# Kernel tuning notes

Measured on AMD Instinct MI355X. Metric: run time of the kernel, lower is better.

The kernel has to match this reference:

```python
import jax, jax.numpy as jnp
import numpy as np

P = 7            # cfg.POOLING_SIZE (= group_size)
N_CLASSES = 21   # PASCAL VOC incl. background
SPATIAL_SCALE = 1.0 / 16.0


def _round_half_up(x):
    # matches C round() for non-negative roi coords (jnp.round is banker's)
    return jnp.floor(x + 0.5)


def psroi_pool(feat, rois, out_dim):
    """Position-sensitive RoI average pooling via integral images.
    feat: [B, out_dim*P*P, H, W]; rois: [N, 5] (batch_idx, x1, y1, x2, y2).
    Returns [N, out_dim, P, P]."""
    B, C, H, W = feat.shape
    # summed-area table, zero-padded: S[b,c,h,w] = sum feat[b,c,:h,:w]
    S = jnp.cumsum(jnp.cumsum(feat, axis=2), axis=3)
    S = jnp.pad(S, ((0, 0), (0, 0), (1, 0), (1, 0)))

    b = rois[:, 0].astype(jnp.int32)
    x1 = _round_half_up(rois[:, 1]) * SPATIAL_SCALE
    y1 = _round_half_up(rois[:, 2]) * SPATIAL_SCALE
    x2 = _round_half_up(rois[:, 3] + 1.0) * SPATIAL_SCALE
    y2 = _round_half_up(rois[:, 4] + 1.0) * SPATIAL_SCALE
    roi_w = jnp.maximum(x2 - x1, 0.1)
    roi_h = jnp.maximum(y2 - y1, 0.1)
    bin_w = roi_w / P
    bin_h = roi_h / P

    g = jnp.arange(P, dtype=feat.dtype)
    hs = jnp.clip(jnp.floor(g[None] * bin_h[:, None] + y1[:, None]), 0, H).astype(jnp.int32)        # [N,P]
    he = jnp.clip(jnp.ceil((g[None] + 1.0) * bin_h[:, None] + y1[:, None]), 0, H).astype(jnp.int32)
    ws = jnp.clip(jnp.floor(g[None] * bin_w[:, None] + x1[:, None]), 0, W).astype(jnp.int32)
    we = jnp.clip(jnp.ceil((g[None] + 1.0) * bin_w[:, None] + x1[:, None]), 0, W).astype(jnp.int32)

    # channel for (ctop, gh, gw) is (ctop*P + gh)*P + gw == arange(C) reshaped
    c = jnp.arange(C, dtype=jnp.int32).reshape(1, out_dim, P, P)
    bi = b[:, None, None, None]
    h0 = hs[:, None, :, None]; h1 = he[:, None, :, None]
    w0 = ws[:, None, None, :]; w1 = we[:, None, None, :]
    # box-sum from integral image -> [N, out_dim, P, P]
    ssum = S[bi, c, h1, w1] - S[bi, c, h0, w1] - S[bi, c, h1, w0] + S[bi, c, h0, w0]

    dh = jnp.maximum(he - hs, 0)[:, None, :, None]
    dw = jnp.maximum(we - ws, 0)[:, None, None, :]
    area = (dh * dw).astype(feat.dtype)
    return jnp.where(area > 0, ssum / jnp.maximum(area, 1.0), 0.0)


def setup_inputs() -> dict:
    key = jax.random.key(0)
    k1, k2, k3, k4, k5 = jax.random.split(key, 5)
    B, Cin, H, W = 4, 2048, 64, 64
    base_feat = jax.random.normal(k1, (B, Cin, H, W), jnp.float32)
    w_conv1 = 0.01 * jax.random.normal(k2, (1024, Cin), jnp.float32)
    w_cls = 0.01 * jax.random.normal(k3, (N_CLASSES * P * P, 1024), jnp.float32)
    w_bbox = 0.001 * jax.random.normal(k4, (4 * N_CLASSES * P * P, 1024), jnp.float32)
    # 300 ROIs per image in image coords (image size = 16*H = 1024)
    n_per = 300
    ka, kb = jax.random.split(k5)
    xy1 = jax.random.uniform(ka, (B * n_per, 2), jnp.float32, 0.0, 900.0)
    wh = jax.random.uniform(kb, (B * n_per, 2), jnp.float32, 16.0, 160.0)
    xy2 = jnp.minimum(xy1 + wh, 1023.0)
    bidx = jnp.repeat(jnp.arange(B, dtype=jnp.float32), n_per)[:, None]
    rois = jnp.concatenate([bidx, xy1[:, 0:1], xy1[:, 1:2], xy2[:, 0:1], xy2[:, 1:2]], axis=1)
    return {"base_feat": base_feat, "rois": rois, "w_conv1": w_conv1, "w_cls": w_cls, "w_bbox": w_bbox}


def reference(base_feat, rois, w_conv1, w_cls, w_bbox):
    B = base_feat.shape[0]
    n_per = rois.shape[0] // B
    # 1x1 conv (no bias) + relu
    x = jax.nn.relu(jnp.einsum('oi,bihw->bohw', w_conv1, base_feat))
    # cls branch: 1x1 conv -> PSRoIPool -> PxP avgpool -> softmax
    cls_feat = jnp.einsum('oi,bihw->bohw', w_cls, x)
    pooled_cls = psroi_pool(cls_feat, rois, N_CLASSES)        # [N, 21, P, P]
    cls_score = pooled_cls.mean(axis=(2, 3))                   # [N, 21]
    cls_prob = jax.nn.softmax(cls_score, axis=1)
    # bbox branch: 1x1 conv -> PSRoIPool -> PxP avgpool
    bbox_feat = jnp.einsum('oi,bihw->bohw', w_bbox, x)
    pooled_loc = psroi_pool(bbox_feat, rois, 4 * N_CLASSES)    # [N, 84, P, P]
    bbox_pred = pooled_loc.mean(axis=(2, 3))                    # [N, 84]
    return cls_prob.reshape(B, n_per, -1), bbox_pred.reshape(B, n_per, -1)
```

## Files before the change

kernel.cpp:

```cpp
#include <hip/hip_runtime.h>
#include <cstdint>


typedef __attribute__((ext_vector_type(8))) short short8;
typedef __attribute__((ext_vector_type(4))) short short4v;
typedef __attribute__((ext_vector_type(4))) float f32x4;

#define OFF_FEATT 0ull
#define OFF_W1    67108864ull
#define OFF_U2    0ull
#define OFF_P2    64225280ull
#define OFF_WC    71303168ull
#define OFF_DESC  84148224ull
#define OFF_SCORE 86155264ull
#define OFF_X     86810624ull
#define OFF_U1    153919488ull
#define OFF_P1    282370048ull
#define ONEPASS_BYTES 296419328ull

__device__ __forceinline__ unsigned short f2bf(float f) {
  unsigned u = __float_as_uint(f);
  u += 0x7fffu + ((u >> 16) & 1u);
  return (unsigned short)(u >> 16);
}
__device__ __forceinline__ float bf2f(unsigned short h) {
  return __uint_as_float(((unsigned)h) << 16);
}

__device__ __forceinline__ int swz6(int k6, int key) {
  return ((((k6 >> 3) & 7) ^ key) << 3) | (k6 & 7);
}

__device__ __forceinline__ void gload16(const void* g, void* l) {
  __builtin_amdgcn_global_load_lds((const __attribute__((address_space(1))) void*)g,
                                   (__attribute__((address_space(3))) void*)l, 16, 0, 0);
}

__global__ __launch_bounds__(256) void k_cvt_w1(const float* __restrict__ src,
                                                unsigned short* __restrict__ dst) {
  int t = blockIdx.x * 256 + threadIdx.x;
  long e = (long)t * 4;
  if (e >= 1024 * 2048) return;
  int o = (int)(e >> 11), k = (int)(e & 2047);
  float4 q = *(const float4*)(src + e);
  short4v s = {(short)f2bf(q.x), (short)f2bf(q.y), (short)f2bf(q.z), (short)f2bf(q.w)};
  int kp = (k & ~63) | swz6(k & 63, o & 7);
  *(short4v*)(dst + (size_t)o * 2048 + kp) = s;
}

__global__ __launch_bounds__(256) void k_cvt_wcomb(const float* __restrict__ wcls,
                                                   const float* __restrict__ wbbox,
                                                   unsigned short* __restrict__ dst) {
  int t = blockIdx.x * 256 + threadIdx.x;
  if (t >= 128 * 49 * 256) return;
  size_t e = (size_t)t * 4;
  int c = (int)(e / 50176);
  int rem = (int)(e - (size_t)c * 50176);
  int ij = rem >> 10, k = rem & 1023;
  float4 q = make_float4(0.f, 0.f, 0.f, 0.f);
  if (c < 21)       q = *(const float4*)(wcls + (size_t)(c * 49 + ij) * 1024 + k);
  else if (c < 105) q = *(const float4*)(wbbox + (size_t)((c - 21) * 49 + ij) * 1024 + k);
  short4v s = {(short)f2bf(q.x), (short)f2bf(q.y), (short)f2bf(q.z), (short)f2bf(q.w)};
  int kp = (k & ~63) | swz6(k & 63, c & 7);
  *(short4v*)(dst + ((size_t)(c * 49 + ij) * 1024 + kp)) = s;
}

__global__ __launch_bounds__(256) void k_tpose(const float* __restrict__ src,
                                               unsigned short* __restrict__ dst) {
  __shared__ float tile[64][65];
  int s0 = blockIdx.x * 64, c0 = blockIdx.y * 64, b = blockIdx.z;
  int tx = threadIdx.x & 63, ty = threadIdx.x >> 6;
  const float* sp = src + ((size_t)b * 2048 + c0) * 4096 + s0;
#pragma unroll
  for (int i = 0; i < 16; i++) {
    int cl = ty * 16 + i;
    tile[cl][tx] = sp[(size_t)cl * 4096 + tx];
  }
  __syncthreads();
  unsigned short* dp = dst + ((size_t)b * 4096 + s0) * 2048 + c0;
  int c4 = (threadIdx.x & 15) * 4;
  int sy = threadIdx.x >> 4;
#pragma unroll
  for (int i = 0; i < 4; i++) {
    int sl = i * 16 + sy;
    int key = sl & 7;
    short4v v = {(short)f2bf(tile[c4 + 0][sl]), (short)f2bf(tile[c4 + 1][sl]),
                 (short)f2bf(tile[c4 + 2][sl]), (short)f2bf(tile[c4 + 3][sl])};
    *(short4v*)(dp + (size_t)sl * 2048 + swz6(c4, key)) = v;
  }
}

__global__ __launch_bounds__(256) void k_gemm_conv1(const short* __restrict__ A,
                                                    const short* __restrict__ Bw,
                                                    float* __restrict__ X) {
  int mt = blockIdx.x, nt = blockIdx.y, b = blockIdx.z;
  __shared__ short As[128 * 64];
  __shared__ short Bs[128 * 64];
  int tid = threadIdx.x, lane = tid & 63, wave = tid >> 6;
  int wm = wave >> 1, wn = wave & 1;
  f32x4 acc[4][4];
#pragma unroll
  for (int i = 0; i < 4; i++)
#pragma unroll
    for (int j = 0; j < 4; j++) acc[i][j] = (f32x4){0.f, 0.f, 0.f, 0.f};

  const short* Ab = A + ((size_t)b * 4096 + (size_t)mt * 128) * 2048;
  const short* Bb = Bw + (size_t)nt * 128 * 2048;
  int lr = lane >> 3;
  int lc = (lane & 7) * 8;
  int key = lane & 7;

  for (int k0 = 0; k0 < 2048; k0 += 64) {
#pragma unroll
    for (int i = 0; i < 4; i++) {
      int row = i * 32 + wave * 8 + lr;
      gload16(Ab + (size_t)row * 2048 + k0 + lc, (char*)As + (i * 32 + wave * 8) * 128);
      gload16(Bb + (size_t)row * 2048 + k0 + lc, (char*)Bs + (i * 32 + wave * 8) * 128);
    }
    __syncthreads();
#pragma unroll
    for (int kt = 0; kt < 2; kt++) {
      int ko = (((kt << 2) | (lane >> 4)) ^ key) << 3;
      short8 af[4], bfr[4];
#pragma unroll
      for (int i = 0; i < 4; i++)
        af[i] = *(const short8*)(As + (wm * 64 + i * 16 + (lane & 15)) * 64 + ko);
#pragma unroll
      for (int j = 0; j < 4; j++)
        bfr[j] = *(const short8*)(Bs + (wn * 64 + j * 16 + (lane & 15)) * 64 + ko);
#pragma unroll
      for (int i = 0; i < 4; i++)
#pragma unroll
        for (int j = 0; j < 4; j++)
          acc[i][j] = __builtin_amdgcn_mfma_f32_16x16x32_bf16(af[i], bfr[j], acc[i][j], 0, 0, 0);
    }
    __syncthreads();
  }
  float* Xb = X + ((size_t)b * 4096 + (size_t)mt * 128) * 1024 + nt * 128;
#pragma unroll
  for (int i = 0; i < 4; i++)
#pragma unroll
    for (int j = 0; j < 4; j++) {
      int row = wm * 64 + i * 16 + (lane >> 4) * 4;
      int col = wn * 64 + j * 16 + (lane & 15);
#pragma unroll
      for (int r = 0; r < 4; r++)
        Xb[(size_t)(row + r) * 1024 + col] = fmaxf(acc[i][j][r], 0.f);
    }
}

__global__ __launch_bounds__(256) void k_desc(const float* __restrict__ rois,
                                              int* __restrict__ desc) {
  int t = blockIdx.x * 256 + threadIdx.x;
  if (t >= 1280 * 49) return;
  int roi = t / 49, ij = t - roi * 49;
  int* d = desc + (size_t)t * 8;
  if (roi >= 1200) { d[0] = 0; d[1] = 0; d[2] = 0; d[3] = 0; d[4] = 0; ((float*)d)[5] = 0.f; return; }
  const float* r = rois + (size_t)roi * 5;
  int b = (int)r[0];
  float x1 = __fmul_rn(floorf(__fadd_rn(r[1], 0.5f)), 0.0625f);
  float y1 = __fmul_rn(floorf(__fadd_rn(r[2], 0.5f)), 0.0625f);
  float x2 = __fmul_rn(floorf(__fadd_rn(__fadd_rn(r[3], 1.0f), 0.5f)), 0.0625f);
  float y2 = __fmul_rn(floorf(__fadd_rn(__fadd_rn(r[4], 1.0f), 0.5f)), 0.0625f);
  float bw = __fdiv_rn(fmaxf(__fsub_rn(x2, x1), 0.1f), 7.0f);
  float bh = __fdiv_rn(fmaxf(__fsub_rn(y2, y1), 0.1f), 7.0f);
  int i = ij / 7, j = ij - (ij / 7) * 7;
  float fi = (float)i, fj = (float)j;
  int hs = (int)fminf(fmaxf(floorf(__fadd_rn(__fmul_rn(fi, bh), y1)), 0.f), 64.f);
  int he = (int)fminf(fmaxf(ceilf(__fadd_rn(__fmul_rn(__fadd_rn(fi, 1.f), bh), y1)), 0.f), 64.f);
  int wsx = (int)fminf(fmaxf(floorf(__fadd_rn(__fmul_rn(fj, bw), x1)), 0.f), 64.f);
  int we = (int)fminf(fmaxf(ceilf(__fadd_rn(__fmul_rn(__fadd_rn(fj, 1.f), bw), x1)), 0.f), 64.f);
  int dh = max(he - hs, 0), dw = max(we - wsx, 0);
  float inv = (dh * dw > 0) ? 1.0f / (float)(dh * dw) : 0.f;
  d[0] = b; d[1] = hs; d[2] = he; d[3] = wsx; d[4] = we;
  ((float*)d)[5] = inv;
}

__global__ __launch_bounds__(256) void k_ubuild(const float* __restrict__ X,
                                                const int* __restrict__ desc,
                                                unsigned short* __restrict__ U) {
  int t = blockIdx.x;
  const int* d = desc + (size_t)t * 8;
  int b = d[0], hs = d[1], he = d[2], wsx = d[3], we = d[4];
  float inv = ((const float*)d)[5];
  int key = (t / 49) & 7;
  int k = threadIdx.x * 4;
  float ax = 0.f, ay = 0.f, az = 0.f, aw = 0.f;
  for (int h = hs; h < he; h++) {
    const float* rowp = X + ((size_t)((b * 64 + h) * 64 + wsx)) * 1024 + k;
    for (int w = wsx; w < we; w++) {
      float4 q = *(const float4*)rowp;
      ax += q.x; ay += q.y; az += q.z; aw += q.w;
      rowp += 1024;
    }
  }
  short4v s = {(short)f2bf(ax * inv), (short)f2bf(ay * inv),
               (short)f2bf(az * inv), (short)f2bf(aw * inv)};
  int kp = (k & ~63) | swz6(k & 63, key);
  *(short4v*)(U + (size_t)t * 1024 + kp) = s;
}

__global__ __launch_bounds__(256) void k_poolgemm2(const unsigned short* __restrict__ U,
                                                   const unsigned short* __restrict__ Wc,
                                                   unsigned short* __restrict__ P,
                                                   int nroi) {
  int mt = blockIdx.x;
  int ij = blockIdx.y;
  __shared__ short As[64 * 64];
  __shared__ short Bs[128 * 64];
  int tid = threadIdx.x, lane = tid & 63, wave = tid >> 6;
  f32x4 acc[4][2];
#pragma unroll
  for (int i = 0; i < 4; i++)
#pragma unroll
    for (int j = 0; j < 2; j++) acc[i][j] = (f32x4){0.f, 0.f, 0.f, 0.f};

  const unsigned short* Ab = U + ((size_t)mt * 64 * 49 + ij) * 1024;
  const unsigned short* Bb = Wc + (size_t)ij * 1024;
  int lr = lane >> 3, lc = (lane & 7) * 8;
  int key = lane & 7;

  for (int k0 = 0; k0 < 1024; k0 += 64) {
#pragma unroll
    for (int i = 0; i < 2; i++) {
      int row = i * 32 + wave * 8 + lr;
      gload16(Ab + (size_t)row * (49 * 1024) + k0 + lc, (char*)As + (i * 32 + wave * 8) * 128);
    }
#pragma unroll
    for (int i = 0; i < 4; i++) {
      int row = i * 32 + wave * 8 + lr;
      gload16(Bb + (size_t)row * (49 * 1024) + k0 + lc, (char*)Bs + (i * 32 + wave * 8) * 128);
    }
    __syncthreads();
#pragma unroll
    for (int kt = 0; kt < 2; kt++) {
      int ko = (((kt << 2) | (lane >> 4)) ^ key) << 3;
      short8 af[4], bfr[2];
#pragma unroll
      for (int i = 0; i < 4; i++)
        af[i] = *(const short8*)(As + (i * 16 + (lane & 15)) * 64 + ko);
#pragma unroll
      for (int j = 0; j < 2; j++)
        bfr[j] = *(const short8*)(Bs + (wave * 32 + j * 16 + (lane & 15)) * 64 + ko);
#pragma unroll
      for (int i = 0; i < 4; i++)
#pragma unroll
        for (int j = 0; j < 2; j++)
          acc[i][j] = __builtin_amdgcn_mfma_f32_16x16x32_bf16(af[i], bfr[j], acc[i][j], 0, 0, 0);
    }
    __syncthreads();
  }
  unsigned short* Pb = P + (size_t)ij * nroi * 112;
#pragma unroll
  for (int i = 0; i < 4; i++)
#pragma unroll
    for (int j = 0; j < 2; j++) {
      int cc = wave * 32 + j * 16 + (lane & 15);
      if (cc < 112) {
        int rbase = mt * 64 + i * 16 + (lane >> 4) * 4;
#pragma unroll
        for (int r = 0; r < 4; r++)
          Pb[(size_t)(rbase + r) * 112 + cc] = f2bf(acc[i][j][r]);
      }
    }
}

__global__ __launch_bounds__(256) void k_reduce(const unsigned short* __restrict__ P,
                                                float* __restrict__ score, int nroi) {
  int t = blockIdx.x * 256 + threadIdx.x;
  if (t >= nroi * 112) return;
  int roi = t / 112, c = t - roi * 112;
  float s = 0.f;
#pragma unroll 7
  for (int ij = 0; ij < 49; ij++) s += bf2f(P[(size_t)ij * nroi * 112 + t]);
  score[(size_t)roi * 128 + c] = s;
}

__global__ __launch_bounds__(256) void k_final(const float* __restrict__ score,
                                               float* __restrict__ out) {
  int t = blockIdx.x * 256 + threadIdx.x;
  if (t < 1200) {
    float s[21];
    float mx = -1e30f;
#pragma unroll
    for (int c = 0; c < 21; c++) {
      s[c] = score[(size_t)t * 128 + c] * (1.f / 49.f);
      mx = fmaxf(mx, s[c]);
    }
    float sum = 0.f;
#pragma unroll
    for (int c = 0; c < 21; c++) { s[c] = expf(s[c] - mx); sum += s[c]; }
    float rs = 1.f / sum;
#pragma unroll
    for (int c = 0; c < 21; c++) out[(size_t)t * 21 + c] = s[c] * rs;
  }
  if (t < 100800) {
    int roi = t / 84, c = t - (t / 84) * 84;
    out[25200 + t] = score[(size_t)roi * 128 + 21 + c] * (1.f / 49.f);
  }
}

extern "C" void kernel_launch(void* const* d_in, const int* in_sizes, int n_in,
                              void* d_out, int out_size, void* d_ws, size_t ws_size,
                              hipStream_t stream) {
  const float* base_feat = (const float*)d_in[0];
  const float* rois      = (const float*)d_in[1];
  const float* w_conv1   = (const float*)d_in[2];
  const float* w_cls     = (const float*)d_in[3];
  const float* w_bbox    = (const float*)d_in[4];
  float* out = (float*)d_out;
  char* ws = (char*)d_ws;

  unsigned short* featT = (unsigned short*)(ws + OFF_FEATT);
  unsigned short* w1b   = (unsigned short*)(ws + OFF_W1);
  unsigned short* Wc    = (unsigned short*)(ws + OFF_WC);
  int*            desc  = (int*)(ws + OFF_DESC);
  float*          score = (float*)(ws + OFF_SCORE);
  float*          X     = (float*)(ws + OFF_X);

  k_cvt_w1<<<2048, 256, 0, stream>>>(w_conv1, w1b);
  k_cvt_wcomb<<<6272, 256, 0, stream>>>(w_cls, w_bbox, Wc);
  k_tpose<<<dim3(64, 32, 4), 256, 0, stream>>>(base_feat, featT);
  k_gemm_conv1<<<dim3(32, 8, 4), 256, 0, stream>>>((const short*)featT, (const short*)w1b, X);
  k_desc<<<245, 256, 0, stream>>>(rois, desc);

  if (ws_size >= ONEPASS_BYTES) {
    unsigned short* U = (unsigned short*)(ws + OFF_U1);
    unsigned short* P = (unsigned short*)(ws + OFF_P1);
    k_ubuild<<<1280 * 49, 256, 0, stream>>>(X, desc, U);
    k_poolgemm2<<<dim3(20, 49), 256, 0, stream>>>(U, Wc, P, 1280);
    k_reduce<<<560, 256, 0, stream>>>(P, score, 1280);
  } else {
    unsigned short* U = (unsigned short*)(ws + OFF_U2);
    unsigned short* P = (unsigned short*)(ws + OFF_P2);
    for (int h = 0; h < 2; h++) {
      k_ubuild<<<640 * 49, 256, 0, stream>>>(X, desc + (size_t)h * 640 * 49 * 8, U);
      k_poolgemm2<<<dim3(10, 49), 256, 0, stream>>>(U, Wc, P, 640);
      k_reduce<<<280, 256, 0, stream>>>(P, score + (size_t)h * 640 * 128, 640);
    }
  }
  k_final<<<394, 256, 0, stream>>>(score, out);
}
```

Measured before the change: 434.6 us.

## Fuse prep kernels, restructure RoI pooling per-RoI, bin-major layouts and fused finalize

The weight conversions and RoI descriptor computation are merged into one prep kernel. The transpose now uses float4 loads and 16-byte stores. The pooling builder processes a whole RoI per block, sharing each row read across the seven column bins. U and Wc are stored bin-major so the pool GEMM reads contiguous rows with 128x128 tiles, and reduce, softmax and output are fused into one kernel. This cuts launches and redundant global reads of X, at the cost of more register pressure and less parallelism in the builder (1280 blocks instead of 62720).

```diff
diff --git a/kernel.cpp b/kernel.cpp
--- a/kernel.cpp
+++ b/kernel.cpp
@@ -7,9 +7,9 @@
 typedef __attribute__((ext_vector_type(4))) float f32x4;
 
 #define OFF_FEATT 0ull
-#define OFF_W1    67108864ull
 #define OFF_U2    0ull
 #define OFF_P2    64225280ull
+#define OFF_W1    67108864ull
 #define OFF_WC    71303168ull
 #define OFF_DESC  84148224ull
 #define OFF_SCORE 86155264ull
@@ -36,122 +36,37 @@
                                    (__attribute__((address_space(3))) void*)l, 16, 0, 0);
 }
 
-__global__ __launch_bounds__(256) void k_cvt_w1(const float* __restrict__ src,
-                                                unsigned short* __restrict__ dst) {
-  int t = blockIdx.x * 256 + threadIdx.x;
-  long e = (long)t * 4;
-  if (e >= 1024 * 2048) return;
-  int o = (int)(e >> 11), k = (int)(e & 2047);
-  float4 q = *(const float4*)(src + e);
-  short4v s = {(short)f2bf(q.x), (short)f2bf(q.y), (short)f2bf(q.z), (short)f2bf(q.w)};
-  int kp = (k & ~63) | swz6(k & 63, o & 7);
-  *(short4v*)(dst + (size_t)o * 2048 + kp) = s;
-}
-
-__global__ __launch_bounds__(256) void k_cvt_wcomb(const float* __restrict__ wcls,
-                                                   const float* __restrict__ wbbox,
-                                                   unsigned short* __restrict__ dst) {
-  int t = blockIdx.x * 256 + threadIdx.x;
-  if (t >= 128 * 49 * 256) return;
-  size_t e = (size_t)t * 4;
-  int c = (int)(e / 50176);
-  int rem = (int)(e - (size_t)c * 50176);
-  int ij = rem >> 10, k = rem & 1023;
-  float4 q = make_float4(0.f, 0.f, 0.f, 0.f);
-  if (c < 21)       q = *(const float4*)(wcls + (size_t)(c * 49 + ij) * 1024 + k);
-  else if (c < 105) q = *(const float4*)(wbbox + (size_t)((c - 21) * 49 + ij) * 1024 + k);
-  short4v s = {(short)f2bf(q.x), (short)f2bf(q.y), (short)f2bf(q.z), (short)f2bf(q.w)};
-  int kp = (k & ~63) | swz6(k & 63, c & 7);
-  *(short4v*)(dst + ((size_t)(c * 49 + ij) * 1024 + kp)) = s;
-}
-
-__global__ __launch_bounds__(256) void k_tpose(const float* __restrict__ src,
-                                               unsigned short* __restrict__ dst) {
-  __shared__ float tile[64][65];
-  int s0 = blockIdx.x * 64, c0 = blockIdx.y * 64, b = blockIdx.z;
-  int tx = threadIdx.x & 63, ty = threadIdx.x >> 6;
-  const float* sp = src + ((size_t)b * 2048 + c0) * 4096 + s0;
-#pragma unroll
-  for (int i = 0; i < 16; i++) {
-    int cl = ty * 16 + i;
-    tile[cl][tx] = sp[(size_t)cl * 4096 + tx];
-  }
-  __syncthreads();
-  unsigned short* dp = dst + ((size_t)b * 4096 + s0) * 2048 + c0;
-  int c4 = (threadIdx.x & 15) * 4;
-  int sy = threadIdx.x >> 4;
-#pragma unroll
-  for (int i = 0; i < 4; i++) {
-    int sl = i * 16 + sy;
-    int key = sl & 7;
-    short4v v = {(short)f2bf(tile[c4 + 0][sl]), (short)f2bf(tile[c4 + 1][sl]),
-                 (short)f2bf(tile[c4 + 2][sl]), (short)f2bf(tile[c4 + 3][sl])};
-    *(short4v*)(dp + (size_t)sl * 2048 + swz6(c4, key)) = v;
-  }
-}
-
-__global__ __launch_bounds__(256) void k_gemm_conv1(const short* __restrict__ A,
-                                                    const short* __restrict__ Bw,
-                                                    float* __restrict__ X) {
-  int mt = blockIdx.x, nt = blockIdx.y, b = blockIdx.z;
-  __shared__ short As[128 * 64];
-  __shared__ short Bs[128 * 64];
-  int tid = threadIdx.x, lane = tid & 63, wave = tid >> 6;
-  int wm = wave >> 1, wn = wave & 1;
-  f32x4 acc[4][4];
-#pragma unroll
-  for (int i = 0; i < 4; i++)
-#pragma unroll
-    for (int j = 0; j < 4; j++) acc[i][j] = (f32x4){0.f, 0.f, 0.f, 0.f};
-
-  const short* Ab = A + ((size_t)b * 4096 + (size_t)mt * 128) * 2048;
-  const short* Bb = Bw + (size_t)nt * 128 * 2048;
-  int lr = lane >> 3;
-  int lc = (lane & 7) * 8;
-  int key = lane & 7;
-
-  for (int k0 = 0; k0 < 2048; k0 += 64) {
-#pragma unroll
-    for (int i = 0; i < 4; i++) {
-      int row = i * 32 + wave * 8 + lr;
-      gload16(Ab + (size_t)row * 2048 + k0 + lc, (char*)As + (i * 32 + wave * 8) * 128);
-      gload16(Bb + (size_t)row * 2048 + k0 + lc, (char*)Bs + (i * 32 + wave * 8) * 128);
-    }
-    __syncthreads();
-#pragma unroll
-    for (int kt = 0; kt < 2; kt++) {
-      int ko = (((kt << 2) | (lane >> 4)) ^ key) << 3;
-      short8 af[4], bfr[4];
-#pragma unroll
-      for (int i = 0; i < 4; i++)
-        af[i] = *(const short8*)(As + (wm * 64 + i * 16 + (lane & 15)) * 64 + ko);
-#pragma unroll
-      for (int j = 0; j < 4; j++)
-        bfr[j] = *(const short8*)(Bs + (wn * 64 + j * 16 + (lane & 15)) * 64 + ko);
-#pragma unroll
-      for (int i = 0; i < 4; i++)
-#pragma unroll
-        for (int j = 0; j < 4; j++)
-          acc[i][j] = __builtin_amdgcn_mfma_f32_16x16x32_bf16(af[i], bfr[j], acc[i][j], 0, 0, 0);
-    }
-    __syncthreads();
-  }
-  float* Xb = X + ((size_t)b * 4096 + (size_t)mt * 128) * 1024 + nt * 128;
-#pragma unroll
-  for (int i = 0; i < 4; i++)
-#pragma unroll
-    for (int j = 0; j < 4; j++) {
-      int row = wm * 64 + i * 16 + (lane >> 4) * 4;
-      int col = wn * 64 + j * 16 + (lane & 15);
-#pragma unroll
-      for (int r = 0; r < 4; r++)
-        Xb[(size_t)(row + r) * 1024 + col] = fmaxf(acc[i][j][r], 0.f);
-    }
-}
-
-__global__ __launch_bounds__(256) void k_desc(const float* __restrict__ rois,
+__global__ __launch_bounds__(256) void k_prep(const float* __restrict__ w1,
+                                              const float* __restrict__ wcls,
+                                              const float* __restrict__ wbbox,
+                                              const float* __restrict__ rois,
+                                              unsigned short* __restrict__ w1b,
+                                              unsigned short* __restrict__ Wc,
                                               int* __restrict__ desc) {
-  int t = blockIdx.x * 256 + threadIdx.x;
+  int bid = blockIdx.x;
+  if (bid < 2048) {
+    long e = ((long)bid * 256 + threadIdx.x) * 4;
+    int o = (int)(e >> 11), k = (int)(e & 2047);
+    float4 q = *(const float4*)(w1 + e);
+    short4v s = {(short)f2bf(q.x), (short)f2bf(q.y), (short)f2bf(q.z), (short)f2bf(q.w)};
+    int kp = (k & ~63) | swz6(k & 63, o & 7);
+    *(short4v*)(w1b + (size_t)o * 2048 + kp) = s;
+    return;
+  }
+  if (bid < 8320) {
+    size_t e = ((size_t)(bid - 2048) * 256 + threadIdx.x) * 4;
+    int c = (int)(e / 50176);
+    int rem = (int)(e - (size_t)c * 50176);
+    int ij = rem >> 10, k = rem & 1023;
+    float4 q = make_float4(0.f, 0.f, 0.f, 0.f);
+    if (c < 21)       q = *(const float4*)(wcls + (size_t)(c * 49 + ij) * 1024 + k);
+    else if (c < 105) q = *(const float4*)(wbbox + (size_t)((c - 21) * 49 + ij) * 1024 + k);
+    short4v s = {(short)f2bf(q.x), (short)f2bf(q.y), (short)f2bf(q.z), (short)f2bf(q.w)};
+    int kp = (k & ~63) | swz6(k & 63, c & 7);
+    *(short4v*)(Wc + ((size_t)(ij * 128 + c) * 1024 + kp)) = s;
+    return;
+  }
+  int t = (bid - 8320) * 256 + threadIdx.x;
   if (t >= 1280 * 49) return;
   int roi = t / 49, ij = t - roi * 49;
   int* d = desc + (size_t)t * 8;
@@ -176,76 +91,180 @@
   ((float*)d)[5] = inv;
 }
 
+__global__ __launch_bounds__(256) void k_tpose(const float* __restrict__ src,
+                                               unsigned short* __restrict__ dst) {
+  __shared__ float tile[64][65];
+  int s0 = blockIdx.x * 64, c0 = blockIdx.y * 64, b = blockIdx.z;
+  int cl = threadIdx.x >> 4;
+  int sv = (threadIdx.x & 15) * 4;
+  const float* sp = src + ((size_t)(b * 2048 + c0)) * 4096 + s0;
+#pragma unroll
+  for (int i = 0; i < 4; i++) {
+    int c = i * 16 + cl;
+    float4 q = *(const float4*)(sp + (size_t)c * 4096 + sv);
+    tile[c][sv + 0] = q.x; tile[c][sv + 1] = q.y;
+    tile[c][sv + 2] = q.z; tile[c][sv + 3] = q.w;
+  }
+  __syncthreads();
+  int s = threadIdx.x >> 2;
+  int cq = (threadIdx.x & 3) * 16;
+  int key = s & 7;
+  unsigned short* dp = dst + ((size_t)(b * 4096 + s0 + s)) * 2048 + c0;
+  float q[16];
+#pragma unroll
+  for (int z = 0; z < 16; z++) q[z] = tile[cq + z][s];
+  short8 v0 = {(short)f2bf(q[0]), (short)f2bf(q[1]), (short)f2bf(q[2]), (short)f2bf(q[3]),
+               (short)f2bf(q[4]), (short)f2bf(q[5]), (short)f2bf(q[6]), (short)f2bf(q[7])};
+  short8 v1 = {(short)f2bf(q[8]), (short)f2bf(q[9]), (short)f2bf(q[10]), (short)f2bf(q[11]),
+               (short)f2bf(q[12]), (short)f2bf(q[13]), (short)f2bf(q[14]), (short)f2bf(q[15])};
+  int ga = cq >> 3;
+  *(short8*)(dp + (((ga + 0) ^ key) << 3)) = v0;
+  *(short8*)(dp + (((ga + 1) ^ key) << 3)) = v1;
+}
+
+__global__ __launch_bounds__(256) void k_gemm_conv1(const short* __restrict__ A,
+                                                    const short* __restrict__ Bw,
+                                                    float* __restrict__ X) {
+  int mt = blockIdx.x, nt = blockIdx.y, b = blockIdx.z;
+  __shared__ short As[128 * 64];
+  __shared__ short Bs[128 * 64];
+  int tid = threadIdx.x, lane = tid & 63, wave = tid >> 6;
+  int wm = wave >> 1, wn = wave & 1;
+  f32x4 acc[4][4];
+#pragma unroll
+  for (int i = 0; i < 4; i++)
+#pragma unroll
+    for (int j = 0; j < 4; j++) acc[i][j] = (f32x4){0.f, 0.f, 0.f, 0.f};
+
+  const short* Ab = A + ((size_t)b * 4096 + (size_t)mt * 128) * 2048;
+  const short* Bb = Bw + (size_t)nt * 128 * 2048;
+  int lr = lane >> 3;
+  int lc = (lane & 7) * 8;
+  int key = lane & 7;
+
+  for (int k0 = 0; k0 < 2048; k0 += 64) {
+#pragma unroll
+    for (int i = 0; i < 4; i++) {
+      int row = i * 32 + wave * 8 + lr;
+      gload16(Ab + (size_t)row * 2048 + k0 + lc, (char*)As + (i * 32 + wave * 8) * 128);
+      gload16(Bb + (size_t)row * 2048 + k0 + lc, (char*)Bs + (i * 32 + wave * 8) * 128);
+    }
+    __syncthreads();
+#pragma unroll
+    for (int kt = 0; kt < 2; kt++) {
+      int ko = (((kt << 2) | (lane >> 4)) ^ key) << 3;
+      short8 af[4], bfr[4];
+#pragma unroll
+      for (int i = 0; i < 4; i++)
+        af[i] = *(const short8*)(As + (wm * 64 + i * 16 + (lane & 15)) * 64 + ko);
+#pragma unroll
+      for (int j = 0; j < 4; j++)
+        bfr[j] = *(const short8*)(Bs + (wn * 64 + j * 16 + (lane & 15)) * 64 + ko);
+#pragma unroll
+      for (int i = 0; i < 4; i++)
+#pragma unroll
+        for (int j = 0; j < 4; j++)
+          acc[i][j] = __builtin_amdgcn_mfma_f32_16x16x32_bf16(af[i], bfr[j], acc[i][j], 0, 0, 0);
+    }
+    __syncthreads();
+  }
+  float* Xb = X + ((size_t)b * 4096 + (size_t)mt * 128) * 1024 + nt * 128;
+#pragma unroll
+  for (int i = 0; i < 4; i++)
+#pragma unroll
+    for (int j = 0; j < 4; j++) {
+      int row = wm * 64 + i * 16 + (lane >> 4) * 4;
+      int col = wn * 64 + j * 16 + (lane & 15);
+#pragma unroll
+      for (int r = 0; r < 4; r++)
+        Xb[(size_t)(row + r) * 1024 + col] = fmaxf(acc[i][j][r], 0.f);
+    }
+}
+
 __global__ __launch_bounds__(256) void k_ubuild(const float* __restrict__ X,
                                                 const int* __restrict__ desc,
-                                                unsigned short* __restrict__ U) {
-  int t = blockIdx.x;
-  const int* d = desc + (size_t)t * 8;
-  int b = d[0], hs = d[1], he = d[2], wsx = d[3], we = d[4];
-  float inv = ((const float*)d)[5];
-  int key = (t / 49) & 7;
+                                                unsigned short* __restrict__ U,
+                                                int nroi) {
+  int lroi = blockIdx.x;
+  const int* db = desc + (size_t)lroi * 49 * 8;
+  int b = db[0];
+  int wsj[7], wej[7];
+#pragma unroll
+  for (int j = 0; j < 7; j++) { wsj[j] = db[j * 8 + 3]; wej[j] = db[j * 8 + 4]; }
+  int wlo = wsj[0], whi = wej[6];
   int k = threadIdx.x * 4;
-  float ax = 0.f, ay = 0.f, az = 0.f, aw = 0.f;
-  for (int h = hs; h < he; h++) {
-    const float* rowp = X + ((size_t)((b * 64 + h) * 64 + wsx)) * 1024 + k;
-    for (int w = wsx; w < we; w++) {
-      float4 q = *(const float4*)rowp;
-      ax += q.x; ay += q.y; az += q.z; aw += q.w;
-      rowp += 1024;
-    }
-  }
-  short4v s = {(short)f2bf(ax * inv), (short)f2bf(ay * inv),
-               (short)f2bf(az * inv), (short)f2bf(aw * inv)};
-  int kp = (k & ~63) | swz6(k & 63, key);
-  *(short4v*)(U + (size_t)t * 1024 + kp) = s;
-}
-
-__global__ __launch_bounds__(256) void k_poolgemm2(const unsigned short* __restrict__ U,
+  const float* Xb = X + (size_t)b * 64 * 64 * 1024 + k;
+  int kp = (k & ~63) | swz6(k & 63, lroi & 7);
+  unsigned short* Ur = U + (size_t)lroi * 1024 + kp;
+  for (int i = 0; i < 7; i++) {
+    int hs = db[(i * 7) * 8 + 1], he = db[(i * 7) * 8 + 2];
+    float ca[7][4];
+#pragma unroll
+    for (int j = 0; j < 7; j++) { ca[j][0] = 0.f; ca[j][1] = 0.f; ca[j][2] = 0.f; ca[j][3] = 0.f; }
+    for (int h = hs; h < he; h++) {
+      const float* rp = Xb + ((size_t)(h * 64 + wlo)) * 1024;
+      for (int w = wlo; w < whi; w++) {
+        float4 q = *(const float4*)rp;
+        rp += 1024;
+#pragma unroll
+        for (int j = 0; j < 7; j++) {
+          if (w >= wsj[j] && w < wej[j]) {
+            ca[j][0] += q.x; ca[j][1] += q.y; ca[j][2] += q.z; ca[j][3] += q.w;
+          }
+        }
+      }
+    }
+#pragma unroll
+    for (int j = 0; j < 7; j++) {
+      float inv = ((const float*)db)[(i * 7 + j) * 8 + 5];
+      short4v s = {(short)f2bf(ca[j][0] * inv), (short)f2bf(ca[j][1] * inv),
+                   (short)f2bf(ca[j][2] * inv), (short)f2bf(ca[j][3] * inv)};
+      *(short4v*)(Ur + (size_t)(i * 7 + j) * nroi * 1024) = s;
+    }
+  }
+}
+
+__global__ __launch_bounds__(256) void k_poolgemm3(const unsigned short* __restrict__ U,
                                                    const unsigned short* __restrict__ Wc,
                                                    unsigned short* __restrict__ P,
                                                    int nroi) {
-  int mt = blockIdx.x;
-  int ij = blockIdx.y;
-  __shared__ short As[64 * 64];
+  int mt = blockIdx.x, ij = blockIdx.y;
+  __shared__ short As[128 * 64];
   __shared__ short Bs[128 * 64];
   int tid = threadIdx.x, lane = tid & 63, wave = tid >> 6;
-  f32x4 acc[4][2];
+  int wm = wave >> 1, wn = wave & 1;
+  f32x4 acc[4][4];
 #pragma unroll
   for (int i = 0; i < 4; i++)
 #pragma unroll
-    for (int j = 0; j < 2; j++) acc[i][j] = (f32x4){0.f, 0.f, 0.f, 0.f};
-
-  const unsigned short* Ab = U + ((size_t)mt * 64 * 49 + ij) * 1024;
-  const unsigned short* Bb = Wc + (size_t)ij * 1024;
-  int lr = lane >> 3, lc = (lane & 7) * 8;
-  int key = lane & 7;
+    for (int j = 0; j < 4; j++) acc[i][j] = (f32x4){0.f, 0.f, 0.f, 0.f};
+
+  const unsigned short* Ab = U + ((size_t)ij * nroi + mt * 128) * 1024;
+  const unsigned short* Bb = Wc + (size_t)ij * 128 * 1024;
+  int lr = lane >> 3, lc = (lane & 7) * 8, key = lane & 7;
 
   for (int k0 = 0; k0 < 1024; k0 += 64) {
-#pragma unroll
-    for (int i = 0; i < 2; i++) {
-      int row = i * 32 + wave * 8 + lr;
-      gload16(Ab + (size_t)row * (49 * 1024) + k0 + lc, (char*)As + (i * 32 + wave * 8) * 128);
-    }
 #pragma unroll
     for (int i = 0; i < 4; i++) {
       int row = i * 32 + wave * 8 + lr;
-      gload16(Bb + (size_t)row * (49 * 1024) + k0 + lc, (char*)Bs + (i * 32 + wave * 8) * 128);
+      gload16(Ab + (size_t)row * 1024 + k0 + lc, (char*)As + (i * 32 + wave * 8) * 128);
+      gload16(Bb + (size_t)row * 1024 + k0 + lc, (char*)Bs + (i * 32 + wave * 8) * 128);
     }
     __syncthreads();
 #pragma unroll
     for (int kt = 0; kt < 2; kt++) {
       int ko = (((kt << 2) | (lane >> 4)) ^ key) << 3;
-      short8 af[4], bfr[2];
+      short8 af[4], bfr[4];
 #pragma unroll
       for (int i = 0; i < 4; i++)
-        af[i] = *(const short8*)(As + (i * 16 + (lane & 15)) * 64 + ko);
-#pragma unroll
-      for (int j = 0; j < 2; j++)
-        bfr[j] = *(const short8*)(Bs + (wave * 32 + j * 16 + (lane & 15)) * 64 + ko);
+        af[i] = *(const short8*)(As + (wm * 64 + i * 16 + (lane & 15)) * 64 + ko);
+#pragma unroll
+      for (int j = 0; j < 4; j++)
+        bfr[j] = *(const short8*)(Bs + (wn * 64 + j * 16 + (lane & 15)) * 64 + ko);
 #pragma unroll
       for (int i = 0; i < 4; i++)
 #pragma unroll
-        for (int j = 0; j < 2; j++)
+        for (int j = 0; j < 4; j++)
           acc[i][j] = __builtin_amdgcn_mfma_f32_16x16x32_bf16(af[i], bfr[j], acc[i][j], 0, 0, 0);
     }
     __syncthreads();
@@ -254,49 +273,44 @@
 #pragma unroll
   for (int i = 0; i < 4; i++)
 #pragma unroll
-    for (int j = 0; j < 2; j++) {
-      int cc = wave * 32 + j * 16 + (lane & 15);
-      if (cc < 112) {
-        int rbase = mt * 64 + i * 16 + (lane >> 4) * 4;
+    for (int j = 0; j < 4; j++) {
+      int col = wn * 64 + j * 16 + (lane & 15);
+      if (col < 112) {
+        int rbase = mt * 128 + wm * 64 + i * 16 + (lane >> 4) * 4;
 #pragma unroll
         for (int r = 0; r < 4; r++)
-          Pb[(size_t)(rbase + r) * 112 + cc] = f2bf(acc[i][j][r]);
+          Pb[(size_t)(rbase + r) * 112 + col] = f2bf(acc[i][j][r]);
       }
     }
 }
 
-__global__ __launch_bounds__(256) void k_reduce(const unsigned short* __restrict__ P,
-                                                float* __restrict__ score, int nroi) {
-  int t = blockIdx.x * 256 + threadIdx.x;
-  if (t >= nroi * 112) return;
-  int roi = t / 112, c = t - roi * 112;
-  float s = 0.f;
+__global__ __launch_bounds__(256) void k_finalize(const unsigned short* __restrict__ P,
+                                                  float* __restrict__ out,
+                                                  int nroi, int roiBase) {
+  __shared__ float sc[2][112];
+  int half = threadIdx.x >> 7, t = threadIdx.x & 127;
+  int lroi = blockIdx.x * 2 + half;
+  int roi = roiBase + lroi;
+  if (t < 112) {
+    float s = 0.f;
 #pragma unroll 7
-  for (int ij = 0; ij < 49; ij++) s += bf2f(P[(size_t)ij * nroi * 112 + t]);
-  score[(size_t)roi * 128 + c] = s;
-}
-
-__global__ __launch_bounds__(256) void k_final(const float* __restrict__ score,
-                                               float* __restrict__ out) {
-  int t = blockIdx.x * 256 + threadIdx.x;
-  if (t < 1200) {
-    float s[21];
-    float mx = -1e30f;
-#pragma unroll
-    for (int c = 0; c < 21; c++) {
-      s[c] = score[(size_t)t * 128 + c] * (1.f / 49.f);
-      mx = fmaxf(mx, s[c]);
-    }
-    float sum = 0.f;
-#pragma unroll
-    for (int c = 0; c < 21; c++) { s[c] = expf(s[c] - mx); sum += s[c]; }
-    float rs = 1.f / sum;
-#pragma unroll
-    for (int c = 0; c < 21; c++) out[(size_t)t * 21 + c] = s[c] * rs;
-  }
-  if (t < 100800) {
-    int roi = t / 84, c = t - (t / 84) * 84;
-    out[25200 + t] = score[(size_t)roi * 128 + 21 + c] * (1.f / 49.f);
+    for (int ij = 0; ij < 49; ij++) s += bf2f(P[((size_t)ij * nroi + lroi) * 112 + t]);
+    sc[half][t] = s;
+  }
+  __syncthreads();
+  if (roi < 1200) {
+    if (t < 21) {
+      float mx = -1e30f;
+#pragma unroll
+      for (int c = 0; c < 21; c++) mx = fmaxf(mx, sc[half][c] * (1.f / 49.f));
+      float sum = 0.f;
+#pragma unroll
+      for (int c = 0; c < 21; c++) sum += expf(sc[half][c] * (1.f / 49.f) - mx);
+      float rs = 1.f / sum;
+      out[(size_t)roi * 21 + t] = expf(sc[half][t] * (1.f / 49.f) - mx) * rs;
+    }
+    if (t < 84)
+      out[25200 + (size_t)roi * 84 + t] = sc[half][21 + t] * (1.f / 49.f);
   }
 }
 
@@ -315,29 +329,25 @@
   unsigned short* w1b   = (unsigned short*)(ws + OFF_W1);
   unsigned short* Wc    = (unsigned short*)(ws + OFF_WC);
   int*            desc  = (int*)(ws + OFF_DESC);
-  float*          score = (float*)(ws + OFF_SCORE);
   float*          X     = (float*)(ws + OFF_X);
 
-  k_cvt_w1<<<2048, 256, 0, stream>>>(w_conv1, w1b);
-  k_cvt_wcomb<<<6272, 256, 0, stream>>>(w_cls, w_bbox, Wc);
+  k_prep<<<8565, 256, 0, stream>>>(w_conv1, w_cls, w_bbox, rois, w1b, Wc, desc);
   k_tpose<<<dim3(64, 32, 4), 256, 0, stream>>>(base_feat, featT);
   k_gemm_conv1<<<dim3(32, 8, 4), 256, 0, stream>>>((const short*)featT, (const short*)w1b, X);
-  k_desc<<<245, 256, 0, stream>>>(rois, desc);
 
   if (ws_size >= ONEPASS_BYTES) {
     unsigned short* U = (unsigned short*)(ws + OFF_U1);
     unsigned short* P = (unsigned short*)(ws + OFF_P1);
-    k_ubuild<<<1280 * 49, 256, 0, stream>>>(X, desc, U);
-    k_poolgemm2<<<dim3(20, 49), 256, 0, stream>>>(U, Wc, P, 1280);
-    k_reduce<<<560, 256, 0, stream>>>(P, score, 1280);
+    k_ubuild<<<1280, 256, 0, stream>>>(X, desc, U, 1280);
+    k_poolgemm3<<<dim3(10, 49), 256, 0, stream>>>(U, Wc, P, 1280);
+    k_finalize<<<640, 256, 0, stream>>>(P, out, 1280, 0);
   } else {
     unsigned short* U = (unsigned short*)(ws + OFF_U2);
     unsigned short* P = (unsigned short*)(ws + OFF_P2);
     for (int h = 0; h < 2; h++) {
-      k_ubuild<<<640 * 49, 256, 0, stream>>>(X, desc + (size_t)h * 640 * 49 * 8, U);
-      k_poolgemm2<<<dim3(10, 49), 256, 0, stream>>>(U, Wc, P, 640);
-      k_reduce<<<280, 256, 0, stream>>>(P, score + (size_t)h * 640 * 128, 640);
-    }
-  }
-  k_final<<<394, 256, 0, stream>>>(score, out);
-}
+      k_ubuild<<<640, 256, 0, stream>>>(X, desc + (size_t)h * 640 * 49 * 8, U, 640);
+      k_poolgemm3<<<dim3(5, 49), 256, 0, stream>>>(U, Wc, P, 640);
+      k_finalize<<<320, 256, 0, stream>>>(P, out, 640, h * 640);
+    }
+  }
+}
```

New measurement: 440.6 us. Within noise of the previous version (+1.4%).
